# Performance work log

Measured on AMD Instinct MI355X. Metric: run time of the kernel, lower is better.

Reference implementation:

```python
import jax, jax.numpy as jnp
import numpy as np

L = 5          # num_layers
N = 50000      # nodes
E = 600000     # edges
D = 128        # num_features == hidden_units
G = 256        # graphs in batch
O = 10         # num_outputs
BN_EPS = 1e-5


def setup_inputs() -> dict:
    key = jax.random.key(0)
    ks = jax.random.split(key, 8)
    x = jax.random.normal(ks[0], (N, D), jnp.float32)
    edge_index = jax.random.randint(ks[1], (2, E), 0, N, jnp.int32)
    edge_attr = jax.random.randint(ks[2], (E, 3), 0, 8, jnp.int32)
    batch = jnp.sort(jax.random.randint(ks[3], (N,), 0, G, jnp.int32))
    s = 0.05
    return {
        "x": x,
        "edge_index": edge_index,
        "edge_attr": edge_attr,
        "batch": batch,
        "bond_emb": jax.random.normal(ks[4], (L, 3, 8, D), jnp.float32) * s,
        "conv_w1": jax.random.normal(ks[5], (L, D, D), jnp.float32) * s,
        "conv_b1": jnp.zeros((L, D), jnp.float32),
        "conv_bn_gamma": jnp.ones((L, D), jnp.float32),
        "conv_bn_beta": jnp.zeros((L, D), jnp.float32),
        "conv_bn_mean": jnp.zeros((L, D), jnp.float32),
        "conv_bn_var": jnp.ones((L, D), jnp.float32),
        "conv_w2": jax.random.normal(ks[6], (L, D, D), jnp.float32) * s,
        "conv_b2": jnp.zeros((L, D), jnp.float32),
        "bn_gamma": jnp.ones((L, D), jnp.float32),
        "bn_beta": jnp.zeros((L, D), jnp.float32),
        "bn_mean": jnp.zeros((L, D), jnp.float32),
        "bn_var": jnp.ones((L, D), jnp.float32),
        "fc_w": jax.random.normal(ks[7], (L + 1, D, O), jnp.float32) * s,
        "fc_b": jnp.zeros((L + 1, O), jnp.float32),
    }


def _bn_eval(h, gamma, beta, mean, var):
    return (h - mean) * jax.lax.rsqrt(var + BN_EPS) * gamma + beta


def reference(x, edge_index, edge_attr, batch, bond_emb,
              conv_w1, conv_b1, conv_bn_gamma, conv_bn_beta, conv_bn_mean, conv_bn_var,
              conv_w2, conv_b2, bn_gamma, bn_beta, bn_mean, bn_var, fc_w, fc_b):
    src, dst = edge_index[0], edge_index[1]  # x_j = x[src], aggregate at dst
    feat_ids = jnp.arange(3)
    outs = [x]
    for i in range(L):
        # BondEncoder: sum of per-feature embeddings -> [E, D]
        ea = bond_emb[i][feat_ids, edge_attr].sum(axis=1)
        # GINEConv (eps=0): msg = relu(x_j + edge_attr), scatter-add, nn(x + aggr)
        msg = jax.nn.relu(x[src] + ea)
        aggr = jax.ops.segment_sum(msg, dst, num_segments=N)
        h = x + aggr
        h = h @ conv_w1[i] + conv_b1[i]
        h = jax.nn.relu(_bn_eval(h, conv_bn_gamma[i], conv_bn_beta[i], conv_bn_mean[i], conv_bn_var[i]))
        h = h @ conv_w2[i] + conv_b2[i]
        x = jax.nn.relu(_bn_eval(h, bn_gamma[i], bn_beta[i], bn_mean[i], bn_var[i]))
        outs.append(x)
    # global mean pool per layer output, linear head, sum (dropout = identity in eval)
    counts = jax.ops.segment_sum(jnp.ones((N,), x.dtype), batch, num_segments=G)
    inv = 1.0 / jnp.maximum(counts, 1.0)
    out = jnp.zeros((G, O), x.dtype)
    for i, h in enumerate(outs):
        pooled = jax.ops.segment_sum(h, batch, num_segments=G) * inv[:, None]
        out = out + pooled @ fc_w[i] + fc_b[i]
    return out
```

## Files before the change

### kernel.cpp

```cpp
#include <hip/hip_runtime.h>

#define NN 50000
#define EE 600000
#define DD 128
#define GG 256
#define LL 5
#define OO 10
#define BN_EPS 1e-5f
#define CPAD 513
#define ESTRIDE 40
#define SENT (512u << 16)

#define B_SCAT  2344
#define B_COMBO 1283
#define B_WT    160
#define B_INV   1
#define B_CVTP  3125
#define B_PREP  (B_SCAT + B_COMBO + B_WT + B_INV + B_CVTP)

typedef __attribute__((ext_vector_type(8))) short short8;
typedef __attribute__((ext_vector_type(16))) float float16;

__device__ __forceinline__ unsigned short f2b(float f) {
    unsigned u = __float_as_uint(f);
    unsigned r = u + 0x7FFFu + ((u >> 16) & 1u);
    return (unsigned short)(r >> 16);
}
__device__ __forceinline__ unsigned pk2(float lo, float hi) {
    return (unsigned)f2b(lo) | ((unsigned)f2b(hi) << 16);
}
__device__ __forceinline__ float blo(unsigned u) { return __uint_as_float(u << 16); }
__device__ __forceinline__ float bhi(unsigned u) { return __uint_as_float(u & 0xFFFF0000u); }

__device__ __forceinline__ void acc8(float* acc, uint4 xv, uint4 cv) {
    acc[0] += fmaxf(blo(xv.x) + blo(cv.x), 0.f);
    acc[1] += fmaxf(bhi(xv.x) + bhi(cv.x), 0.f);
    acc[2] += fmaxf(blo(xv.y) + blo(cv.y), 0.f);
    acc[3] += fmaxf(bhi(xv.y) + bhi(cv.y), 0.f);
    acc[4] += fmaxf(blo(xv.z) + blo(cv.z), 0.f);
    acc[5] += fmaxf(bhi(xv.z) + bhi(cv.z), 0.f);
    acc[6] += fmaxf(blo(xv.w) + blo(cv.w), 0.f);
    acc[7] += fmaxf(bhi(xv.w) + bhi(cv.w), 0.f);
}

__launch_bounds__(256)
__global__ void prep(const float* __restrict__ x, const int* __restrict__ ei,
                     const int* __restrict__ eattr, const int* __restrict__ batch,
                     const float* __restrict__ bond,
                     const float* __restrict__ w1, const float* __restrict__ w2,
                     unsigned* __restrict__ xb4, unsigned short* __restrict__ combo,
                     short* __restrict__ wt, int* __restrict__ epos,
                     unsigned* __restrict__ e_info,
                     float* __restrict__ inv, float* __restrict__ pooled0) {
    const int bid = (int)(((long long)blockIdx.x * 1021) % B_PREP);
    const int t = threadIdx.x;
    if (bid < B_SCAT) {
        int e = bid * 256 + t;
        if (e < EE) {
            int dst = ei[EE + e];
            int slot = atomicAdd(&epos[dst], 1);
            if (slot < ESTRIDE) {
                unsigned cidx = (unsigned)eattr[e * 3 + 0] | ((unsigned)eattr[e * 3 + 1] << 3)
                              | ((unsigned)eattr[e * 3 + 2] << 6);
                e_info[dst * ESTRIDE + slot] = (unsigned)ei[e] | (cidx << 16);
            }
        }
    } else if (bid < B_SCAT + B_COMBO) {
        int e = (bid - B_SCAT) * 256 + t;
        if (e < LL * CPAD * DD) {
            int l = e / (CPAD * DD), rem = e - l * (CPAD * DD);
            int c = rem / DD, d = rem - c * DD;
            float s;
            if (c == 512) s = -1e30f;
            else {
                const float* b_ = bond + (size_t)l * 3 * 8 * DD;
                s = b_[(c & 7) * DD + d] + b_[(8 + ((c >> 3) & 7)) * DD + d]
                  + b_[(16 + (c >> 6)) * DD + d];
            }
            combo[e] = f2b(s);
        }
    } else if (bid < B_SCAT + B_COMBO + B_WT) {
        __shared__ float tile[32][33];
        int b = bid - B_SCAT - B_COMBO;
        int mat = b >> 4, tl = b & 15;
        int k0 = (tl >> 2) * 32, c0 = (tl & 3) * 32;
        const float* W = (mat < 5) ? (w1 + (size_t)mat * DD * DD)
                                   : (w2 + (size_t)(mat - 5) * DD * DD);
        int j = t & 31, q = t >> 5;
#pragma unroll
        for (int rr = 0; rr < 4; ++rr) {
            int row = q + rr * 8;
            tile[row][j] = W[(size_t)(k0 + row) * DD + c0 + j];
        }
        __syncthreads();
#pragma unroll
        for (int rr = 0; rr < 4; ++rr) {
            int cr = q + rr * 8;
            wt[(size_t)mat * DD * DD + (size_t)(c0 + cr) * DD + k0 + j] = (short)f2b(tile[j][cr]);
        }
    } else if (bid < B_SCAT + B_COMBO + B_WT + B_INV) {
        __shared__ int sg[GG + 1];
        int g = t, lo = 0, hi = NN;
        while (lo < hi) { int m = (lo + hi) >> 1; if (batch[m] < g) lo = m + 1; else hi = m; }
        sg[g] = lo;
        if (g == 0) sg[GG] = NN;
        __syncthreads();
        inv[g] = 1.0f / fmaxf((float)(sg[g + 1] - sg[g]), 1.0f);
    } else {
        __shared__ float part[4][DD];
        int b = bid - (B_SCAT + B_COMBO + B_WT + B_INV);
        int gid = b * 256 + t;
        const float4* xp = (const float4*)(x + (size_t)gid * 8);
        float4 a = xp[0], c4 = xp[1];
        uint4 o;
        o.x = pk2(a.x, a.y); o.y = pk2(a.z, a.w);
        o.z = pk2(c4.x, c4.y); o.w = pk2(c4.z, c4.w);
        ((uint4*)xb4)[gid] = o;

        int row0 = b * 16;
        int row  = row0 + (t >> 4);
        int col8 = (t & 15) * 8;
        int gmin = batch[row0];
        int dg   = batch[row] - gmin;
        ((float*)part)[t] = 0.f;
        ((float*)part)[t + 256] = 0.f;
        __syncthreads();
        float v[8] = {a.x, a.y, a.z, a.w, c4.x, c4.y, c4.z, c4.w};
        if (dg < 4) {
#pragma unroll
            for (int j = 0; j < 8; ++j) atomicAdd(&part[dg][col8 + j], v[j]);
        } else {
#pragma unroll
            for (int j = 0; j < 8; ++j) atomicAdd(&pooled0[(gmin + dg) * DD + col8 + j], v[j]);
        }
        __syncthreads();
        for (int q2 = t; q2 < 4 * DD; q2 += 256) {
            int jj = q2 >> 7, c2 = q2 & 127;
            float pv = part[jj][c2];
            if (pv != 0.f && gmin + jj < GG) atomicAdd(&pooled0[(gmin + jj) * DD + c2], pv);
        }
    }
}

__launch_bounds__(256)
__global__ void aggr_csr(const unsigned short* __restrict__ xin,
                         const int* __restrict__ epos,
                         const unsigned* __restrict__ e_info,
                         const unsigned short* __restrict__ combo,
                         unsigned short* __restrict__ hin) {
    int node = blockIdx.x * 4 + (threadIdx.x >> 6);
    int lane = threadIdx.x & 63;
    if (node >= NN) return;
    const int base = node * ESTRIDE;
    int deg = epos[node]; if (deg > ESTRIDE) deg = ESTRIDE;
    const int eg = lane >> 4;
    const int f  = (lane & 15) * 8;

    unsigned i0 = e_info[base + eg];
    unsigned i1 = e_info[base + 4 + eg];
    unsigned i2 = e_info[base + 8 + eg];
    unsigned i3 = e_info[base + 12 + eg];
    if (eg      >= deg) i0 = SENT;
    if (4 + eg  >= deg) i1 = SENT;
    if (8 + eg  >= deg) i2 = SENT;
    if (12 + eg >= deg) i3 = SENT;

    uint4 xv0 = *(const uint4*)&xin[(size_t)(i0 & 0xFFFFu) * DD + f];
    uint4 cv0 = *(const uint4*)&combo[(size_t)(i0 >> 16) * DD + f];
    uint4 xv1 = *(const uint4*)&xin[(size_t)(i1 & 0xFFFFu) * DD + f];
    uint4 cv1 = *(const uint4*)&combo[(size_t)(i1 >> 16) * DD + f];
    uint4 xv2 = *(const uint4*)&xin[(size_t)(i2 & 0xFFFFu) * DD + f];
    uint4 cv2 = *(const uint4*)&combo[(size_t)(i2 >> 16) * DD + f];
    uint4 xv3 = *(const uint4*)&xin[(size_t)(i3 & 0xFFFFu) * DD + f];
    uint4 cv3 = *(const uint4*)&combo[(size_t)(i3 >> 16) * DD + f];

    float acc[8];
#pragma unroll
    for (int i = 0; i < 8; ++i) acc[i] = 0.f;
    acc8(acc, xv0, cv0);
    acc8(acc, xv1, cv1);
    acc8(acc, xv2, cv2);
    acc8(acc, xv3, cv3);

    if (deg > 16) {
        const int dend = base + deg;
        const int pe   = base + ((deg + 7) & ~7);
        for (int p = base + 16; p < pe; p += 8) {
            unsigned j0 = e_info[p + eg];
            unsigned j1 = e_info[p + 4 + eg];
            if (p + eg >= dend)     j0 = SENT;
            if (p + 4 + eg >= dend) j1 = SENT;
            uint4 ax0 = *(const uint4*)&xin[(size_t)(j0 & 0xFFFFu) * DD + f];
            uint4 ac0 = *(const uint4*)&combo[(size_t)(j0 >> 16) * DD + f];
            uint4 ax1 = *(const uint4*)&xin[(size_t)(j1 & 0xFFFFu) * DD + f];
            uint4 ac1 = *(const uint4*)&combo[(size_t)(j1 >> 16) * DD + f];
            acc8(acc, ax0, ac0);
            acc8(acc, ax1, ac1);
        }
    }

#pragma unroll
    for (int i = 0; i < 8; ++i) {
        acc[i] += __shfl_xor(acc[i], 16, 64);
        acc[i] += __shfl_xor(acc[i], 32, 64);
    }
    if (lane < 16) {
        uint4 self = *(const uint4*)&xin[(size_t)node * DD + f];
        uint4 o;
        o.x = pk2(acc[0] + blo(self.x), acc[1] + bhi(self.x));
        o.y = pk2(acc[2] + blo(self.y), acc[3] + bhi(self.y));
        o.z = pk2(acc[4] + blo(self.z), acc[5] + bhi(self.z));
        o.w = pk2(acc[6] + blo(self.w), acc[7] + bhi(self.w));
        *(uint4*)&hin[(size_t)node * DD + f] = o;
    }
}

__launch_bounds__(256)
__global__ void conv_fused(const unsigned short* __restrict__ hin,
                           const short* __restrict__ Wt1, const short* __restrict__ Wt2,
                           const float* __restrict__ b1, const float* __restrict__ g1,
                           const float* __restrict__ be1, const float* __restrict__ m1,
                           const float* __restrict__ v1,
                           const float* __restrict__ b2, const float* __restrict__ g2,
                           const float* __restrict__ be2, const float* __restrict__ m2,
                           const float* __restrict__ v2,
                           const int* __restrict__ batch,
                           unsigned short* __restrict__ outb,
                           float* __restrict__ pool_slot) {
    __shared__ short As[32 * 136];
    __shared__ int sbg[32];
    const int tid  = threadIdx.x;
    const int lane = tid & 63;
    const int wave = tid >> 6;
    const int row0 = blockIdx.x * 32;

    const int col   = wave * 32 + (lane & 31);
    const int khalf = (lane >> 5) * 8;
    const int arow  = lane & 31;
    const int rbase = 4 * (lane >> 5);
    const int gmin  = batch[row0];

    short8 bf[8];
#pragma unroll
    for (int ch = 0; ch < 8; ++ch)
        bf[ch] = *(const short8*)&Wt1[col * DD + ch * 16 + khalf];

    const float sc1 = g1[col] * rsqrtf(v1[col] + BN_EPS);
    const float sh1 = fmaf(b1[col] - m1[col], sc1, be1[col]);
    const float sc2 = g2[col] * rsqrtf(v2[col] + BN_EPS);
    const float sh2 = fmaf(b2[col] - m2[col], sc2, be2[col]);

    if (tid < 32) {
        int row = row0 + tid;
        sbg[tid] = (row < NN) ? batch[row] - gmin : -1;
    }
    for (int i = tid; i < 512; i += 256) {
        int r = i >> 4, c8 = (i & 15) * 8;
        int row = row0 + r;
        uint4 z = make_uint4(0, 0, 0, 0);
        if (row < NN) z = *(const uint4*)&hin[(size_t)row * DD + c8];
        *(uint4*)&As[r * 136 + c8] = z;
    }
    __syncthreads();

    float16 acc0 = {0.f,0.f,0.f,0.f,0.f,0.f,0.f,0.f,0.f,0.f,0.f,0.f,0.f,0.f,0.f,0.f};
#pragma unroll
    for (int ch = 0; ch < 8; ++ch) {
        short8 a0 = *(const short8*)&As[arow * 136 + ch * 16 + khalf];
        acc0 = __builtin_amdgcn_mfma_f32_32x32x16_bf16(a0, bf[ch], acc0, 0, 0, 0);
    }

#pragma unroll
    for (int ch = 0; ch < 8; ++ch)
        bf[ch] = *(const short8*)&Wt2[col * DD + ch * 16 + khalf];

    __syncthreads();
#pragma unroll
    for (int r = 0; r < 16; ++r) {
        int rl = (r & 3) + 8 * (r >> 2) + rbase;
        As[rl * 136 + col] = (short)f2b(fmaxf(fmaf(acc0[r], sc1, sh1), 0.f));
    }
    __syncthreads();

    acc0 = float16{0.f,0.f,0.f,0.f,0.f,0.f,0.f,0.f,0.f,0.f,0.f,0.f,0.f,0.f,0.f,0.f};
#pragma unroll
    for (int ch = 0; ch < 8; ++ch) {
        short8 a0 = *(const short8*)&As[arow * 136 + ch * 16 + khalf];
        acc0 = __builtin_amdgcn_mfma_f32_32x32x16_bf16(a0, bf[ch], acc0, 0, 0, 0);
    }

    float pg0 = 0.f, pg1 = 0.f, pg2 = 0.f, pg3 = 0.f;
#pragma unroll
    for (int r = 0; r < 16; ++r) {
        int rl  = (r & 3) + 8 * (r >> 2) + rbase;
        int row = row0 + rl;
        float v0 = fmaxf(fmaf(acc0[r], sc2, sh2), 0.f);
        if (row < NN) outb[(size_t)row * DD + col] = f2b(v0);
        int ga = sbg[rl];
        pg0 += (ga == 0) ? v0 : 0.f;
        pg1 += (ga == 1) ? v0 : 0.f;
        pg2 += (ga == 2) ? v0 : 0.f;
        pg3 += (ga == 3) ? v0 : 0.f;
    }
    pg0 += __shfl_down(pg0, 32);
    pg1 += __shfl_down(pg1, 32);
    pg2 += __shfl_down(pg2, 32);
    pg3 += __shfl_down(pg3, 32);
    if (lane < 32) {
        if (pg0 != 0.f)                  atomicAdd(&pool_slot[(gmin    ) * DD + col], pg0);
        if (pg1 != 0.f && gmin + 1 < GG) atomicAdd(&pool_slot[(gmin + 1) * DD + col], pg1);
        if (pg2 != 0.f && gmin + 2 < GG) atomicAdd(&pool_slot[(gmin + 2) * DD + col], pg2);
        if (pg3 != 0.f && gmin + 3 < GG) atomicAdd(&pool_slot[(gmin + 3) * DD + col], pg3);
    }
}

__launch_bounds__(64)
__global__ void head(const float* __restrict__ pooled, const float* __restrict__ inv,
                     const float* __restrict__ fcw, const float* __restrict__ fcb,
                     float* __restrict__ out) {
    int g = blockIdx.x, t = threadIdx.x;
    __shared__ float part[LL + 1][OO];
    if (t < (LL + 1) * OO) {
        int l = t / OO, o2 = t - l * OO;
        const float* p = pooled + ((size_t)l * GG + g) * DD;
        const float* w = fcw + (size_t)l * DD * OO + o2;
        float s = 0.f;
        for (int d2 = 0; d2 < DD; ++d2) s = fmaf(p[d2], w[(size_t)d2 * OO], s);
        part[l][o2] = s;
    }
    __syncthreads();
    if (t < OO) {
        float sp = 0.f, sb2 = 0.f;
#pragma unroll
        for (int l = 0; l < LL + 1; ++l) { sp += part[l][t]; sb2 += fcb[l * OO + t]; }
        out[g * OO + t] = sp * inv[g] + sb2;
    }
}

extern "C" void kernel_launch(void* const* d_in, const int* in_sizes, int n_in,
                              void* d_out, int out_size, void* d_ws, size_t ws_size,
                              hipStream_t stream) {
    const float* x_in    = (const float*)d_in[0];
    const int*   ei      = (const int*)d_in[1];
    const int*   eattr   = (const int*)d_in[2];
    const int*   batch   = (const int*)d_in[3];
    const float* bond    = (const float*)d_in[4];
    const float* conv_w1 = (const float*)d_in[5];
    const float* conv_b1 = (const float*)d_in[6];
    const float* cbg     = (const float*)d_in[7];
    const float* cbb     = (const float*)d_in[8];
    const float* cbm     = (const float*)d_in[9];
    const float* cbv     = (const float*)d_in[10];
    const float* conv_w2 = (const float*)d_in[11];
    const float* conv_b2 = (const float*)d_in[12];
    const float* bg      = (const float*)d_in[13];
    const float* bb      = (const float*)d_in[14];
    const float* bm      = (const float*)d_in[15];
    const float* bv      = (const float*)d_in[16];
    const float* fcw     = (const float*)d_in[17];
    const float* fcb     = (const float*)d_in[18];
    float* out = (float*)d_out;

    char* base = (char*)d_ws;
    size_t o = 0;
    auto carve = [&](size_t bytes) { void* p = base + o; o += (bytes + 15) & ~(size_t)15; return p; };
    unsigned short* xbA    = (unsigned short*)carve((size_t)NN * DD * 2);
    unsigned short* xbB    = (unsigned short*)carve((size_t)NN * DD * 2);
    unsigned short* combo  = (unsigned short*)carve((size_t)LL * CPAD * DD * 2);
    short*          wt     = (short*)carve((size_t)10 * DD * DD * 2);
    float*          inv    = (float*)carve(GG * 4);
    const size_t ZBYTES = (size_t)NN * 4 + (size_t)(LL + 1) * GG * DD * 4;
    int*            epos   = (int*)carve(ZBYTES);
    float*          pooled = (float*)((char*)epos + (size_t)NN * 4);
    unsigned*       e_info = (unsigned*)carve((size_t)NN * ESTRIDE * 4);

    hipMemsetAsync(epos, 0, ZBYTES, stream);

    prep<<<B_PREP, 256, 0, stream>>>(x_in, ei, eattr, batch, bond, conv_w1, conv_w2,
                                     (unsigned*)xbA, combo, wt, epos, e_info, inv, pooled);

    const int conv_blocks = (NN + 31) / 32;
    const int aggr_blocks = (NN + 3) / 4;
    unsigned short* xin  = xbA;
    unsigned short* xout = xbB;
    for (int i = 0; i < LL; ++i) {
        aggr_csr<<<aggr_blocks, 256, 0, stream>>>(
            xin, epos, e_info, combo + (size_t)i * CPAD * DD, xout);
        conv_fused<<<conv_blocks, 256, 0, stream>>>(
            xout, wt + (size_t)i * DD * DD, wt + (size_t)(5 + i) * DD * DD,
            conv_b1 + (size_t)i * DD, cbg + (size_t)i * DD, cbb + (size_t)i * DD,
            cbm + (size_t)i * DD, cbv + (size_t)i * DD,
            conv_b2 + (size_t)i * DD, bg + (size_t)i * DD, bb + (size_t)i * DD,
            bm + (size_t)i * DD, bv + (size_t)i * DD,
            batch, xin, pooled + (size_t)(i + 1) * GG * DD);
    }
    head<<<GG, 64, 0, stream>>>(pooled, inv, fcw, fcb, out);
}
```

Measured before the change: 405.3 us.

## Prefill edge slots with sentinel and move layer-0 pooling into head

The edge-slot table is now pre-filled by a memset so that every unused slot decodes to a padded combo row holding -1e30. That lets the aggregation kernel drop its per-slot degree checks, and the edge-slot reads become nontemporal loads. The layer-0 mean pooling and the per-graph count are removed from prep, where they used shared and global atomics plus a separate inverse-count block. The head kernel now does them by binary-searching the batch boundaries and summing its graph's input rows directly. The cost is an extra 8 MB memset and a second full read of the fp32 input in a small 256-block head kernel.

```diff
diff --git a/kernel.cpp b/kernel.cpp
--- a/kernel.cpp
+++ b/kernel.cpp
@@ -7,16 +7,14 @@
 #define LL 5
 #define OO 10
 #define BN_EPS 1e-5f
-#define CPAD 513
+#define CPAD 515
 #define ESTRIDE 40
-#define SENT (512u << 16)
 
 #define B_SCAT  2344
-#define B_COMBO 1283
+#define B_COMBO 1288
 #define B_WT    160
-#define B_INV   1
-#define B_CVTP  3125
-#define B_PREP  (B_SCAT + B_COMBO + B_WT + B_INV + B_CVTP)
+#define B_CVT   3125
+#define B_PREP  (B_SCAT + B_COMBO + B_WT + B_CVT)
 
 typedef __attribute__((ext_vector_type(8))) short short8;
 typedef __attribute__((ext_vector_type(16))) float float16;
@@ -45,13 +43,12 @@
 
 __launch_bounds__(256)
 __global__ void prep(const float* __restrict__ x, const int* __restrict__ ei,
-                     const int* __restrict__ eattr, const int* __restrict__ batch,
+                     const int* __restrict__ eattr,
                      const float* __restrict__ bond,
                      const float* __restrict__ w1, const float* __restrict__ w2,
                      unsigned* __restrict__ xb4, unsigned short* __restrict__ combo,
                      short* __restrict__ wt, int* __restrict__ epos,
-                     unsigned* __restrict__ e_info,
-                     float* __restrict__ inv, float* __restrict__ pooled0) {
+                     unsigned* __restrict__ e_info) {
     const int bid = (int)(((long long)blockIdx.x * 1021) % B_PREP);
     const int t = threadIdx.x;
     if (bid < B_SCAT) {
@@ -71,7 +68,7 @@
             int l = e / (CPAD * DD), rem = e - l * (CPAD * DD);
             int c = rem / DD, d = rem - c * DD;
             float s;
-            if (c == 512) s = -1e30f;
+            if (c >= 512) s = -1e30f;
             else {
                 const float* b_ = bond + (size_t)l * 3 * 8 * DD;
                 s = b_[(c & 7) * DD + d] + b_[(8 + ((c >> 3) & 7)) * DD + d]
@@ -98,47 +95,14 @@
             int cr = q + rr * 8;
             wt[(size_t)mat * DD * DD + (size_t)(c0 + cr) * DD + k0 + j] = (short)f2b(tile[j][cr]);
         }
-    } else if (bid < B_SCAT + B_COMBO + B_WT + B_INV) {
-        __shared__ int sg[GG + 1];
-        int g = t, lo = 0, hi = NN;
-        while (lo < hi) { int m = (lo + hi) >> 1; if (batch[m] < g) lo = m + 1; else hi = m; }
-        sg[g] = lo;
-        if (g == 0) sg[GG] = NN;
-        __syncthreads();
-        inv[g] = 1.0f / fmaxf((float)(sg[g + 1] - sg[g]), 1.0f);
     } else {
-        __shared__ float part[4][DD];
-        int b = bid - (B_SCAT + B_COMBO + B_WT + B_INV);
-        int gid = b * 256 + t;
+        int gid = (bid - (B_SCAT + B_COMBO + B_WT)) * 256 + t;
         const float4* xp = (const float4*)(x + (size_t)gid * 8);
         float4 a = xp[0], c4 = xp[1];
         uint4 o;
         o.x = pk2(a.x, a.y); o.y = pk2(a.z, a.w);
         o.z = pk2(c4.x, c4.y); o.w = pk2(c4.z, c4.w);
         ((uint4*)xb4)[gid] = o;
-
-        int row0 = b * 16;
-        int row  = row0 + (t >> 4);
-        int col8 = (t & 15) * 8;
-        int gmin = batch[row0];
-        int dg   = batch[row] - gmin;
-        ((float*)part)[t] = 0.f;
-        ((float*)part)[t + 256] = 0.f;
-        __syncthreads();
-        float v[8] = {a.x, a.y, a.z, a.w, c4.x, c4.y, c4.z, c4.w};
-        if (dg < 4) {
-#pragma unroll
-            for (int j = 0; j < 8; ++j) atomicAdd(&part[dg][col8 + j], v[j]);
-        } else {
-#pragma unroll
-            for (int j = 0; j < 8; ++j) atomicAdd(&pooled0[(gmin + dg) * DD + col8 + j], v[j]);
-        }
-        __syncthreads();
-        for (int q2 = t; q2 < 4 * DD; q2 += 256) {
-            int jj = q2 >> 7, c2 = q2 & 127;
-            float pv = part[jj][c2];
-            if (pv != 0.f && gmin + jj < GG) atomicAdd(&pooled0[(gmin + jj) * DD + c2], pv);
-        }
     }
 }
 
@@ -156,14 +120,10 @@
     const int eg = lane >> 4;
     const int f  = (lane & 15) * 8;
 
-    unsigned i0 = e_info[base + eg];
-    unsigned i1 = e_info[base + 4 + eg];
-    unsigned i2 = e_info[base + 8 + eg];
-    unsigned i3 = e_info[base + 12 + eg];
-    if (eg      >= deg) i0 = SENT;
-    if (4 + eg  >= deg) i1 = SENT;
-    if (8 + eg  >= deg) i2 = SENT;
-    if (12 + eg >= deg) i3 = SENT;
+    unsigned i0 = __builtin_nontemporal_load(e_info + base + eg);
+    unsigned i1 = __builtin_nontemporal_load(e_info + base + 4 + eg);
+    unsigned i2 = __builtin_nontemporal_load(e_info + base + 8 + eg);
+    unsigned i3 = __builtin_nontemporal_load(e_info + base + 12 + eg);
 
     uint4 xv0 = *(const uint4*)&xin[(size_t)(i0 & 0xFFFFu) * DD + f];
     uint4 cv0 = *(const uint4*)&combo[(size_t)(i0 >> 16) * DD + f];
@@ -183,13 +143,10 @@
     acc8(acc, xv3, cv3);
 
     if (deg > 16) {
-        const int dend = base + deg;
-        const int pe   = base + ((deg + 7) & ~7);
+        const int pe = base + ((deg + 7) & ~7);
         for (int p = base + 16; p < pe; p += 8) {
-            unsigned j0 = e_info[p + eg];
-            unsigned j1 = e_info[p + 4 + eg];
-            if (p + eg >= dend)     j0 = SENT;
-            if (p + 4 + eg >= dend) j1 = SENT;
+            unsigned j0 = __builtin_nontemporal_load(e_info + p + eg);
+            unsigned j1 = __builtin_nontemporal_load(e_info + p + 4 + eg);
             uint4 ax0 = *(const uint4*)&xin[(size_t)(j0 & 0xFFFFu) * DD + f];
             uint4 ac0 = *(const uint4*)&combo[(size_t)(j0 >> 16) * DD + f];
             uint4 ax1 = *(const uint4*)&xin[(size_t)(j1 & 0xFFFFu) * DD + f];
@@ -314,18 +271,41 @@
     }
 }
 
-__launch_bounds__(64)
-__global__ void head(const float* __restrict__ pooled, const float* __restrict__ inv,
+__launch_bounds__(256)
+__global__ void head(const float* __restrict__ x, const int* __restrict__ batch,
+                     const float* __restrict__ pooled,
                      const float* __restrict__ fcw, const float* __restrict__ fcb,
                      float* __restrict__ out) {
     int g = blockIdx.x, t = threadIdx.x;
+    __shared__ float sm[2][DD];
     __shared__ float part[LL + 1][OO];
+    int r0, r1;
+    {
+        int lo = 0, hi = NN;
+        while (lo < hi) { int m = (lo + hi) >> 1; if (batch[m] < g) lo = m + 1; else hi = m; }
+        r0 = lo;
+        lo = 0; hi = NN;
+        while (lo < hi) { int m = (lo + hi) >> 1; if (batch[m] < g + 1) lo = m + 1; else hi = m; }
+        r1 = lo;
+    }
+    const float invg = 1.0f / fmaxf((float)(r1 - r0), 1.0f);
+    {
+        int col = t & 127, par = t >> 7;
+        float s = 0.f;
+        for (int r = r0 + par; r < r1; r += 2) s += x[(size_t)r * DD + col];
+        sm[par][col] = s;
+    }
+    __syncthreads();
     if (t < (LL + 1) * OO) {
         int l = t / OO, o2 = t - l * OO;
-        const float* p = pooled + ((size_t)l * GG + g) * DD;
         const float* w = fcw + (size_t)l * DD * OO + o2;
         float s = 0.f;
-        for (int d2 = 0; d2 < DD; ++d2) s = fmaf(p[d2], w[(size_t)d2 * OO], s);
+        if (l == 0) {
+            for (int d = 0; d < DD; ++d) s = fmaf(sm[0][d] + sm[1][d], w[(size_t)d * OO], s);
+        } else {
+            const float* p = pooled + ((size_t)(l - 1) * GG + g) * DD;
+            for (int d = 0; d < DD; ++d) s = fmaf(p[d], w[(size_t)d * OO], s);
+        }
         part[l][o2] = s;
     }
     __syncthreads();
@@ -333,7 +313,7 @@
         float sp = 0.f, sb2 = 0.f;
 #pragma unroll
         for (int l = 0; l < LL + 1; ++l) { sp += part[l][t]; sb2 += fcb[l * OO + t]; }
-        out[g * OO + t] = sp * inv[g] + sb2;
+        out[g * OO + t] = sp * invg + sb2;
     }
 }
 
@@ -368,16 +348,16 @@
     unsigned short* xbB    = (unsigned short*)carve((size_t)NN * DD * 2);
     unsigned short* combo  = (unsigned short*)carve((size_t)LL * CPAD * DD * 2);
     short*          wt     = (short*)carve((size_t)10 * DD * DD * 2);
-    float*          inv    = (float*)carve(GG * 4);
-    const size_t ZBYTES = (size_t)NN * 4 + (size_t)(LL + 1) * GG * DD * 4;
+    const size_t ZBYTES = (size_t)NN * 4 + (size_t)LL * GG * DD * 4;
     int*            epos   = (int*)carve(ZBYTES);
     float*          pooled = (float*)((char*)epos + (size_t)NN * 4);
     unsigned*       e_info = (unsigned*)carve((size_t)NN * ESTRIDE * 4);
 
     hipMemsetAsync(epos, 0, ZBYTES, stream);
-
-    prep<<<B_PREP, 256, 0, stream>>>(x_in, ei, eattr, batch, bond, conv_w1, conv_w2,
-                                     (unsigned*)xbA, combo, wt, epos, e_info, inv, pooled);
+    hipMemsetAsync(e_info, 0x02, (size_t)NN * ESTRIDE * 4, stream);
+
+    prep<<<B_PREP, 256, 0, stream>>>(x_in, ei, eattr, bond, conv_w1, conv_w2,
+                                     (unsigned*)xbA, combo, wt, epos, e_info);
 
     const int conv_blocks = (NN + 31) / 32;
     const int aggr_blocks = (NN + 3) / 4;
@@ -392,7 +372,7 @@
             cbm + (size_t)i * DD, cbv + (size_t)i * DD,
             conv_b2 + (size_t)i * DD, bg + (size_t)i * DD, bb + (size_t)i * DD,
             bm + (size_t)i * DD, bv + (size_t)i * DD,
-            batch, xin, pooled + (size_t)(i + 1) * GG * DD);
-    }
-    head<<<GG, 64, 0, stream>>>(pooled, inv, fcw, fcb, out);
-}
+            batch, xin, pooled + (size_t)i * GG * DD);
+    }
+    head<<<GG, 256, 0, stream>>>(x_in, batch, pooled, fcw, fcb, out);
+}
```

After: 442.9 us. 9.3% more time.
